# Kernel tuning notes

Hardware: AMD Instinct MI355X
Metric: run time of the kernel (lower is better)

Reference implementation:

```python
import jax, jax.numpy as jnp
import numpy as np

N = 50000      # nodes
E = 800000     # edges (avg degree 16)
IN = 128       # in_feats
H = 8          # num_heads
EMB = 32       # attention embedding dim (mode != 'cross')
OUT = 16       # out_feats per head
EF = 7         # edge (bond) feature dim


def setup_inputs() -> dict:
    key = jax.random.key(0)
    ks = jax.random.split(key, 12)
    s = 0.05  # xavier-ish scale
    return {
        "feat": jax.random.normal(ks[0], (N, IN), jnp.float32),
        "bond": jax.random.uniform(ks[1], (E, EF), jnp.float32),
        "src": jax.random.randint(ks[2], (E,), 0, N, jnp.int32),
        "dst": jax.random.randint(ks[3], (E,), 0, N, jnp.int32),
        "Wq": jax.random.normal(ks[4], (IN, H * EMB), jnp.float32) * s,
        "Wk": jax.random.normal(ks[5], (IN, H * EMB), jnp.float32) * s,
        "Wv": jax.random.normal(ks[6], (IN, H * OUT), jnp.float32) * s,
        "Wek": jax.random.normal(ks[7], (EF, H * EMB), jnp.float32) * s,
        "bek": jnp.zeros((H * EMB,), jnp.float32),
        "Wefc": jax.random.normal(ks[8], (EF, H * OUT), jnp.float32) * s,
        "befc": jnp.zeros((H * OUT,), jnp.float32),
        "bias": jnp.zeros((H * OUT,), jnp.float32),
    }


def reference(feat, bond, src, dst, Wq, Wk, Wv, Wek, bek, Wefc, befc, bias):
    n = feat.shape[0]
    # node projections
    q = (feat @ Wq).reshape(n, H, EMB)      # query
    k = (feat @ Wk).reshape(n, H, EMB)      # key
    v = (feat @ Wv).reshape(n, H, OUT)      # ft (values)
    # per-edge key from bond features
    ek = (bond @ Wek + bek).reshape(-1, H, EMB)
    # mode 'add': e = sum((q[u] + k[v]) * edge_key) over embedding dim  -> [E, H]
    e = ((q[src] + k[dst]) * ek).sum(axis=-1)
    # edge_softmax: segment softmax over incoming edges per destination node
    m = jax.ops.segment_max(e, dst, num_segments=n)          # [N, H]
    ex = jnp.exp(e - m[dst])
    denom = jax.ops.segment_sum(ex, dst, num_segments=n)     # [N, H]
    a = ex / denom[dst]                                      # [E, H]
    # per-edge feature projection
    ef = (bond @ Wefc + befc).reshape(-1, H, OUT)
    # message = ft[src] * edge_feat * a, aggregated by sum at dst
    msg = v[src] * ef * a[:, :, None]                        # [E, H, OUT]
    rst = jax.ops.segment_sum(msg, dst, num_segments=n)      # [N, H, OUT]
    rst = rst + bias.reshape(1, H, OUT)
    return rst
```

## Files before the change

kernel.cpp:

```cpp
#include <hip/hip_runtime.h>
#include <hip/hip_bf16.h>

#define HD   8
#define EMBD 32
#define OUTF 16
#define EFD  7
#define INFD 128
#define QKD  256
#define VOD  128
#define GQD  64
#define CAPMAX 64
#define NB   8
#define MAXSLOT 512
#define PBROW 524

typedef __attribute__((ext_vector_type(8))) short short8;
typedef __attribute__((ext_vector_type(4))) float f32x4;

__device__ __forceinline__ float b2f(unsigned short u) {
    return __uint_as_float(((unsigned int)u) << 16);
}
__device__ __forceinline__ unsigned short f2b(float f) {
    __hip_bfloat16 h = __float2bfloat16(f);
    return __builtin_bit_cast(unsigned short, h);
}
__device__ __forceinline__ unsigned short f2h(float f) {
    return __builtin_bit_cast(unsigned short, (_Float16)f);
}
__device__ __forceinline__ float h2f(unsigned short u) {
    return (float)__builtin_bit_cast(_Float16, u);
}

__global__ __launch_bounds__(256) void setup_kernel(
    const float* __restrict__ Wq, const float* __restrict__ Wk,
    const float* __restrict__ Wv, const float* __restrict__ Wek,
    const float* __restrict__ bek, unsigned short* __restrict__ GwT,
    int* __restrict__ counts, int N)
{
    const int b = blockIdx.x, t = threadIdx.x;
    if (b >= 16) {
        int i = (b - 16) * 256 + t;
        int stride = (gridDim.x - 16) * 256;
        for (; i < N; i += stride) counts[i] = 0;
        return;
    }
    if (b >= 8) {
        #pragma unroll
        for (int k = 0; k < 8; k++) {
            int i = (b - 8) * 2048 + k * 256 + t;
            int r = i >> 7, c = i & 127;
            GwT[(size_t)(128 + c) * 128 + r] = f2b(Wv[(size_t)r * VOD + c]);
        }
        return;
    }
    __shared__ float sWek[EFD * QKD];
    __shared__ float sbek[QKD];
    for (int i = t; i < EFD * QKD; i += 256) sWek[i] = Wek[i];
    for (int i = t; i < QKD; i += 256) sbek[i] = bek[i];
    __syncthreads();

    const int p = b * 256 + t;
    const int side = p >> 10;
    const int r = (p >> 3) & 127;
    const int h = p & 7;
    const float* W = side ? Wk : Wq;
    float wrow[EMBD];
    #pragma unroll
    for (int d = 0; d < EMBD; d++) wrow[d] = W[(size_t)r * QKD + h * EMBD + d];
    #pragma unroll
    for (int f = 0; f < EFD; f++) {
        float m = 0.f;
        #pragma unroll
        for (int d = 0; d < EMBD; d++) m += wrow[d] * sWek[f * QKD + h * EMBD + d];
        GwT[(size_t)(side * 64 + h * 8 + f) * 128 + r] = f2b(m);
    }
    float mb = 0.f;
    #pragma unroll
    for (int d = 0; d < EMBD; d++) mb += wrow[d] * sbek[h * EMBD + d];
    GwT[(size_t)(side * 64 + h * 8 + 7) * 128 + r] = f2b(mb);
}

__global__ __launch_bounds__(256) void work_kernel(
    const float* __restrict__ feat, const unsigned short* __restrict__ GwT,
    unsigned short* __restrict__ gq, unsigned short* __restrict__ gk,
    unsigned short* __restrict__ v_bf, int M,
    const int* __restrict__ src, const int* __restrict__ dst,
    const float* __restrict__ bond, int E,
    int* __restrict__ counts, short8* __restrict__ edata, int cap, int pg)
{
    if ((int)blockIdx.x >= pg) {
        int i = (blockIdx.x - pg) * 256 + threadIdx.x;
        int stride = (gridDim.x - pg) * 256;
        for (; i < E; i += stride) {
            int d = dst[i];
            const float* bp = bond + (size_t)i * EFD;
            short8 rec;
            rec[0] = (short)(unsigned short)src[i];
            #pragma unroll
            for (int f = 0; f < EFD; f++) rec[1 + f] = (short)f2b(bp[f]);
            int p = atomicAdd(&counts[d], 1);
            if (p < cap) edata[(size_t)d * cap + p] = rec;
        }
        return;
    }
    const int wave = threadIdx.x >> 6, lane = threadIdx.x & 63;
    const int quad = lane >> 4, l16 = lane & 15;
    const int m0 = blockIdx.x * 64 + wave * 16;
    const int mrow = m0 + l16;
    const int arow = (mrow < M) ? mrow : 0;

    f32x4 acc[16];
    #pragma unroll
    for (int ct = 0; ct < 16; ct++) acc[ct] = (f32x4){0.f, 0.f, 0.f, 0.f};

    #pragma unroll
    for (int ks = 0; ks < 4; ks++) {
        const float* fp = feat + (size_t)arow * INFD + ks * 32 + quad * 8;
        float4 f0 = *(const float4*)(fp);
        float4 f1 = *(const float4*)(fp + 4);
        short8 a;
        a[0] = (short)f2b(f0.x); a[1] = (short)f2b(f0.y);
        a[2] = (short)f2b(f0.z); a[3] = (short)f2b(f0.w);
        a[4] = (short)f2b(f1.x); a[5] = (short)f2b(f1.y);
        a[6] = (short)f2b(f1.z); a[7] = (short)f2b(f1.w);
        #pragma unroll
        for (int ct = 0; ct < 16; ct++) {
            short8 b = *(const short8*)(GwT + (size_t)(ct * 16 + l16) * 128 + ks * 32 + quad * 8);
            acc[ct] = __builtin_amdgcn_mfma_f32_16x16x32_bf16(a, b, acc[ct], 0, 0, 0);
        }
    }

    const int mt = m0 + quad * 4;
    #pragma unroll
    for (int ct = 0; ct < 16; ct++) {
        int nn = ct * 16 + l16;
        unsigned short* outp; int nc, ldo;
        if (ct < 4)      { outp = gq;   nc = nn;       ldo = GQD; }
        else if (ct < 8) { outp = gk;   nc = nn - 64;  ldo = GQD; }
        else             { outp = v_bf; nc = nn - 128; ldo = VOD; }
        #pragma unroll
        for (int r = 0; r < 4; r++) {
            int mm = mt + r;
            if (mm < M) outp[(size_t)mm * ldo + nc] = f2b(acc[ct][r]);
        }
    }
}

__global__ __launch_bounds__(256) void aggregate_kernel(
    const short8* __restrict__ edata,
    const unsigned short* __restrict__ gq,
    const unsigned short* __restrict__ gk,
    const unsigned short* __restrict__ v_bf,
    const int* __restrict__ counts,
    const float* __restrict__ Wefc,
    const float* __restrict__ befc,
    const float* __restrict__ bias,
    float* __restrict__ out, int N, int cap)
{
    __shared__ __align__(16) unsigned short sBond[MAXSLOT][8];
    __shared__ __align__(8)  unsigned short sS[MAXSLOT];
    __shared__ unsigned char sNode[MAXSLOT];
    __shared__ __align__(16) unsigned short sGK[NB * GQD];
    __shared__ __align__(16) unsigned short sPh[8 * PBROW];
    __shared__ float sL[NB * 8];
    __shared__ int sCnt[NB], sR16[NB], sBase[NB], sTot;

    const int t  = threadIdx.x;
    const int n0 = blockIdx.x * NB;
    const int wv = t >> 6;
    const int l  = t & 63;
    const int lrow = l & 15;
    const int lhi  = l >> 4;
    const int c0 = wv * 32 + 2 * lrow;
    const int h0 = c0 >> 4;

    short8 Bfr[2]; float bout[2];
    #pragma unroll
    for (int j = 0; j < 2; j++) {
        short8 b = {0,0,0,0,0,0,0,0};
        float bo = 0.f;
        if (lhi == 0) {
            const int c = c0 + j;
            #pragma unroll
            for (int f = 0; f < EFD; f++) b[f] = (short)f2b(Wefc[f * VOD + c]);
            b[7] = (short)f2b(befc[c]);
            bo = bias[c];
        }
        Bfr[j] = b; bout[j] = bo;
    }

    if (t < 64) {
        int c = 0;
        if (t < NB) {
            int n = n0 + t;
            c = (n < N) ? min(counts[n], cap) : 0;
        }
        int r16 = (c + 15) & ~15;
        int pre = 0;
        #pragma unroll
        for (int j = 0; j < NB; j++) {
            int vj = __shfl(r16, j, 64);
            pre += (j < t) ? vj : 0;
        }
        if (t < NB) {
            sCnt[t] = c; sR16[t] = r16; sBase[t] = pre;
            if (t == NB - 1) sTot = pre + r16;
        }
    }
    {
        const unsigned gi = (unsigned)n0 * 32u + (unsigned)t;
        if (gi < (unsigned)N * 32u)
            ((unsigned*)sGK)[t] = ((const unsigned*)gk)[gi];
    }
    __syncthreads();

    const int tot = sTot;
    {
        const int b1 = sBase[1], b2 = sBase[2], b3 = sBase[3], b4 = sBase[4],
                  b5 = sBase[5], b6 = sBase[6], b7 = sBase[7];
        for (int i = t; i < tot; i += 256) {
            int nn = (i >= b1) + (i >= b2) + (i >= b3) + (i >= b4)
                   + (i >= b5) + (i >= b6) + (i >= b7);
            int el = i - sBase[nn];
            int cnt = sCnt[nn];
            unsigned short sv = 0;
            short8 st = {0,0,0,0,0,0,0,0};
            if (el < cnt) {
                short8 r = edata[(size_t)(n0 + nn) * cap + el];
                sv = (unsigned short)r[0];
                #pragma unroll
                for (int f = 0; f < EFD; f++) st[f] = r[1 + f];
                st[7] = (short)0x3F80;
            }
            sS[i] = sv;
            sNode[i] = (unsigned char)nn;
            *(short8*)&sBond[i][0] = st;
        }
    }
    __syncthreads();

    for (int idx = t; idx < tot * 8; idx += 256) {
        const int sl = idx >> 3, lh = idx & 7;
        short8 bb = *(const short8*)&sBond[sl][0];
        float ex = 0.f;
        if (bb[7]) {
            const int nn = sNode[sl];
            short8 gv = *(const short8*)(gq + (size_t)sS[sl] * GQD + lh * 8);
            short8 kb = *(const short8*)&sGK[nn * GQD + lh * 8];
            float lv = b2f((unsigned short)gv[7]) + b2f((unsigned short)kb[7]);
            #pragma unroll
            for (int f = 0; f < EFD; f++)
                lv += b2f((unsigned short)bb[f]) *
                      (b2f((unsigned short)gv[f]) + b2f((unsigned short)kb[f]));
            ex = __expf(lv);
        }
        sPh[lh * PBROW + sl] = f2h(ex);
    }
    __syncthreads();

    {
        const int nn = t >> 5, h = (t >> 2) & 7, sub = t & 3;
        const int base = sBase[nn], cnt = sCnt[nn];
        float s = 0.f;
        for (int e = sub; e < cnt; e += 4)
            s += h2f(sPh[h * PBROW + base + e]);
        s += __shfl_xor(s, 1, 64);
        s += __shfl_xor(s, 2, 64);
        if (sub == 0) sL[nn * 8 + h] = s;
    }
    __syncthreads();

    for (int nn = 0; nn < NB; nn++) {
        const int n = n0 + nn;
        if (n >= N) break;
        const int r16 = sR16[nn];
        const int sb  = sBase[nn];
        float a0 = 0.f, a1 = 0.f;
        for (int mt = 0; mt < (r16 >> 4); mt++) {
            short8 A = {0,0,0,0,0,0,0,0};
            if (lhi == 0) A = *(const short8*)&sBond[sb + mt * 16 + lrow][0];
            const int e0 = sb + mt * 16 + lhi * 4;
            const unsigned long long sw = *(const unsigned long long*)&sS[e0];
            const unsigned s0 = (unsigned)(sw & 0xffff), s1 = (unsigned)((sw >> 16) & 0xffff);
            const unsigned s2 = (unsigned)((sw >> 32) & 0xffff), s3 = (unsigned)(sw >> 48);
            const unsigned long long pw = *(const unsigned long long*)&sPh[h0 * PBROW + e0];
            const float p0 = h2f((unsigned short)(pw & 0xffff));
            const float p1 = h2f((unsigned short)((pw >> 16) & 0xffff));
            const float p2 = h2f((unsigned short)((pw >> 32) & 0xffff));
            const float p3 = h2f((unsigned short)(pw >> 48));
            const unsigned w0 = *(const unsigned*)(v_bf + s0 * VOD + c0);
            const unsigned w1 = *(const unsigned*)(v_bf + s1 * VOD + c0);
            const unsigned w2 = *(const unsigned*)(v_bf + s2 * VOD + c0);
            const unsigned w3 = *(const unsigned*)(v_bf + s3 * VOD + c0);
            const f32x4 C0 = __builtin_amdgcn_mfma_f32_16x16x32_bf16(
                A, Bfr[0], (f32x4){0.f, 0.f, 0.f, 0.f}, 0, 0, 0);
            const f32x4 C1 = __builtin_amdgcn_mfma_f32_16x16x32_bf16(
                A, Bfr[1], (f32x4){0.f, 0.f, 0.f, 0.f}, 0, 0, 0);
            a0 = fmaf(p0 * C0[0], __uint_as_float(w0 << 16), a0);
            a1 = fmaf(p0 * C1[0], __uint_as_float(w0 & 0xffff0000u), a1);
            a0 = fmaf(p1 * C0[1], __uint_as_float(w1 << 16), a0);
            a1 = fmaf(p1 * C1[1], __uint_as_float(w1 & 0xffff0000u), a1);
            a0 = fmaf(p2 * C0[2], __uint_as_float(w2 << 16), a0);
            a1 = fmaf(p2 * C1[2], __uint_as_float(w2 & 0xffff0000u), a1);
            a0 = fmaf(p3 * C0[3], __uint_as_float(w3 << 16), a0);
            a1 = fmaf(p3 * C1[3], __uint_as_float(w3 & 0xffff0000u), a1);
        }
        a0 += __shfl_xor(a0, 16, 64);
        a0 += __shfl_xor(a0, 32, 64);
        a1 += __shfl_xor(a1, 16, 64);
        a1 += __shfl_xor(a1, 32, 64);
        if (lhi == 0) {
            const float L = sL[nn * 8 + h0];
            const float iv = (L > 0.f) ? 1.f / L : 0.f;
            float2 o;
            o.x = a0 * iv + bout[0];
            o.y = a1 * iv + bout[1];
            *(float2*)&out[(size_t)n * VOD + c0] = o;
        }
    }
}

extern "C" void kernel_launch(void* const* d_in, const int* in_sizes, int n_in,
                              void* d_out, int out_size, void* d_ws, size_t ws_size,
                              hipStream_t stream) {
    const float* feat = (const float*)d_in[0];
    const float* bond = (const float*)d_in[1];
    const int* src  = (const int*)d_in[2];
    const int* dst  = (const int*)d_in[3];
    const float* Wq   = (const float*)d_in[4];
    const float* Wk   = (const float*)d_in[5];
    const float* Wv   = (const float*)d_in[6];
    const float* Wek  = (const float*)d_in[7];
    const float* bek  = (const float*)d_in[8];
    const float* Wefc = (const float*)d_in[9];
    const float* befc = (const float*)d_in[10];
    const float* bias = (const float*)d_in[11];

    const int N = in_sizes[0] / INFD;
    const int E = in_sizes[2];

    size_t off = 0;
    auto carve = [&](size_t bytes) -> void* {
        void* p = (char*)d_ws + off;
        off += (bytes + 255) & ~(size_t)255;
        return p;
    };
    unsigned short* GwT  = (unsigned short*)carve((size_t)256 * 128 * 2);
    unsigned short* gq   = (unsigned short*)carve((size_t)N * GQD * 2);
    unsigned short* gk   = (unsigned short*)carve((size_t)N * GQD * 2);
    unsigned short* v_bf = (unsigned short*)carve((size_t)N * VOD * 2);
    int* counts    = (int*)carve((size_t)N * 4);

    size_t remain = (ws_size > off) ? (ws_size - off) : 0;
    int cap = (int)(remain / ((size_t)N * 16));
    if (cap > 64) cap = 64;
    if (cap > CAPMAX) cap = CAPMAX;
    if (cap < 1) cap = 1;
    short8* edata = (short8*)carve((size_t)N * cap * 16);

    setup_kernel<<<80, 256, 0, stream>>>(Wq, Wk, Wv, Wek, bek, GwT, counts, N);

    const int pg = (N + 63) / 64;
    work_kernel<<<pg + 3072, 256, 0, stream>>>(feat, GwT, gq, gk, v_bf, N,
                                               src, dst, bond, E, counts, edata, cap, pg);

    aggregate_kernel<<<(N + NB - 1) / NB, 256, 0, stream>>>(
        edata, gq, gk, v_bf, counts, Wefc, befc, bias, (float*)d_out, N, cap);
}
```

Before: 254.2 us.

## Partition edge scatter by XCC-owned destination ranges with dynamic chunk queues

Each scatter block reads its XCC id from a hardware register and works through 8 destination-node ranges, starting with the range tied to its own XCC. Within a range it takes edge chunks from a per-range atomic work pointer and handles only edges whose destination falls in that range. The goal is to keep atomics and writes to counts and edata local to one XCC's L2, cutting cross-die coherence traffic. The cost is that every edge's dst is read 8 times, plus extra work-pointer atomics and block-level syncs.

```diff
diff --git a/kernel.cpp b/kernel.cpp
--- a/kernel.cpp
+++ b/kernel.cpp
@@ -13,6 +13,9 @@
 #define NB   8
 #define MAXSLOT 512
 #define PBROW 524
+#define SCB  2048
+#define CHUNK 2048
+#define XCC_GETREG_IMM (20 | (31 << 11))
 
 typedef __attribute__((ext_vector_type(8))) short short8;
 typedef __attribute__((ext_vector_type(4))) float f32x4;
@@ -35,13 +38,13 @@
     const float* __restrict__ Wq, const float* __restrict__ Wk,
     const float* __restrict__ Wv, const float* __restrict__ Wek,
     const float* __restrict__ bek, unsigned short* __restrict__ GwT,
-    int* __restrict__ counts, int N)
+    int* __restrict__ counts, int NZ)
 {
     const int b = blockIdx.x, t = threadIdx.x;
     if (b >= 16) {
         int i = (b - 16) * 256 + t;
         int stride = (gridDim.x - 16) * 256;
-        for (; i < N; i += stride) counts[i] = 0;
+        for (; i < NZ; i += stride) counts[i] = 0;
         return;
     }
     if (b >= 8) {
@@ -86,20 +89,35 @@
     unsigned short* __restrict__ v_bf, int M,
     const int* __restrict__ src, const int* __restrict__ dst,
     const float* __restrict__ bond, int E,
-    int* __restrict__ counts, short8* __restrict__ edata, int cap, int pg)
+    int* __restrict__ counts, int* __restrict__ workPtr,
+    short8* __restrict__ edata, int cap, int pg)
 {
     if ((int)blockIdx.x >= pg) {
-        int i = (blockIdx.x - pg) * 256 + threadIdx.x;
-        int stride = (gridDim.x - pg) * 256;
-        for (; i < E; i += stride) {
-            int d = dst[i];
-            const float* bp = bond + (size_t)i * EFD;
-            short8 rec;
-            rec[0] = (short)(unsigned short)src[i];
-            #pragma unroll
-            for (int f = 0; f < EFD; f++) rec[1 + f] = (short)f2b(bp[f]);
-            int p = atomicAdd(&counts[d], 1);
-            if (p < cap) edata[(size_t)d * cap + p] = rec;
+        __shared__ int sChunk;
+        unsigned xcc = (unsigned)__builtin_amdgcn_s_getreg(XCC_GETREG_IMM) & 7u;
+        for (int qi = 0; qi < 8; qi++) {
+            const int q  = (int)((xcc + (unsigned)qi) & 7u);
+            const int lo = (int)(((long long)q * M) >> 3);
+            const int hi = (int)(((long long)(q + 1) * M) >> 3);
+            while (true) {
+                if (threadIdx.x == 0) sChunk = atomicAdd(&workPtr[q], CHUNK);
+                __syncthreads();
+                const int base = sChunk;
+                __syncthreads();
+                if (base >= E) break;
+                const int end = (base + CHUNK < E) ? base + CHUNK : E;
+                for (int i = base + (int)threadIdx.x; i < end; i += 256) {
+                    int d = dst[i];
+                    if (d < lo || d >= hi) continue;
+                    const float* bp = bond + (size_t)i * EFD;
+                    short8 rec;
+                    rec[0] = (short)(unsigned short)src[i];
+                    #pragma unroll
+                    for (int f = 0; f < EFD; f++) rec[1 + f] = (short)f2b(bp[f]);
+                    int p = atomicAdd(&counts[d], 1);
+                    if (p < cap) edata[(size_t)d * cap + p] = rec;
+                }
+            }
         }
         return;
     }
@@ -349,7 +367,8 @@
     unsigned short* gq   = (unsigned short*)carve((size_t)N * GQD * 2);
     unsigned short* gk   = (unsigned short*)carve((size_t)N * GQD * 2);
     unsigned short* v_bf = (unsigned short*)carve((size_t)N * VOD * 2);
-    int* counts    = (int*)carve((size_t)N * 4);
+    int* counts    = (int*)carve((size_t)(N + 64) * 4);
+    int* workPtr   = counts + N;
 
     size_t remain = (ws_size > off) ? (ws_size - off) : 0;
     int cap = (int)(remain / ((size_t)N * 16));
@@ -358,11 +377,12 @@
     if (cap < 1) cap = 1;
     short8* edata = (short8*)carve((size_t)N * cap * 16);
 
-    setup_kernel<<<80, 256, 0, stream>>>(Wq, Wk, Wv, Wek, bek, GwT, counts, N);
+    setup_kernel<<<80, 256, 0, stream>>>(Wq, Wk, Wv, Wek, bek, GwT, counts, N + 64);
 
     const int pg = (N + 63) / 64;
-    work_kernel<<<pg + 3072, 256, 0, stream>>>(feat, GwT, gq, gk, v_bf, N,
-                                               src, dst, bond, E, counts, edata, cap, pg);
+    work_kernel<<<pg + SCB, 256, 0, stream>>>(feat, GwT, gq, gk, v_bf, N,
+                                              src, dst, bond, E, counts, workPtr,
+                                              edata, cap, pg);
 
     aggregate_kernel<<<(N + NB - 1) / NB, 256, 0, stream>>>(
         edata, gq, gk, v_bf, counts, Wefc, befc, bias, (float*)d_out, N, cap);
```

Measured after the change: 443.7 us. 74.5% more time.

## Fuse attention logit and softmax denominator into aggregation MFMA loop

Applied to the files above, without the earlier changes.

Drops the separate shared-memory phases that computed per-edge exp logits into an fp16 buffer and reduced per-node denominators. Each lane now recomputes the exp logit for its head inside the main aggregation loop, gathering gq rows directly, and accumulates the denominator alongside the message sums. This removes two block barriers and about 8KB of LDS, and keeps the exp values in fp32 instead of fp16. In exchange, each logit is recomputed by the 16 lanes that share a head, and the gq gathers are repeated across those lanes.

```diff
diff --git a/kernel.cpp b/kernel.cpp
--- a/kernel.cpp
+++ b/kernel.cpp
@@ -12,7 +12,7 @@
 #define CAPMAX 64
 #define NB   8
 #define MAXSLOT 512
-#define PBROW 524
+#define SCB  3072
 
 typedef __attribute__((ext_vector_type(8))) short short8;
 typedef __attribute__((ext_vector_type(4))) float f32x4;
@@ -23,12 +23,6 @@
 __device__ __forceinline__ unsigned short f2b(float f) {
     __hip_bfloat16 h = __float2bfloat16(f);
     return __builtin_bit_cast(unsigned short, h);
-}
-__device__ __forceinline__ unsigned short f2h(float f) {
-    return __builtin_bit_cast(unsigned short, (_Float16)f);
-}
-__device__ __forceinline__ float h2f(unsigned short u) {
-    return (float)__builtin_bit_cast(_Float16, u);
 }
 
 __global__ __launch_bounds__(256) void setup_kernel(
@@ -159,10 +153,7 @@
 {
     __shared__ __align__(16) unsigned short sBond[MAXSLOT][8];
     __shared__ __align__(8)  unsigned short sS[MAXSLOT];
-    __shared__ unsigned char sNode[MAXSLOT];
     __shared__ __align__(16) unsigned short sGK[NB * GQD];
-    __shared__ __align__(16) unsigned short sPh[8 * PBROW];
-    __shared__ float sL[NB * 8];
     __shared__ int sCnt[NB], sR16[NB], sBase[NB], sTot;
 
     const int t  = threadIdx.x;
@@ -233,40 +224,8 @@
                 st[7] = (short)0x3F80;
             }
             sS[i] = sv;
-            sNode[i] = (unsigned char)nn;
             *(short8*)&sBond[i][0] = st;
         }
-    }
-    __syncthreads();
-
-    for (int idx = t; idx < tot * 8; idx += 256) {
-        const int sl = idx >> 3, lh = idx & 7;
-        short8 bb = *(const short8*)&sBond[sl][0];
-        float ex = 0.f;
-        if (bb[7]) {
-            const int nn = sNode[sl];
-            short8 gv = *(const short8*)(gq + (size_t)sS[sl] * GQD + lh * 8);
-            short8 kb = *(const short8*)&sGK[nn * GQD + lh * 8];
-            float lv = b2f((unsigned short)gv[7]) + b2f((unsigned short)kb[7]);
-            #pragma unroll
-            for (int f = 0; f < EFD; f++)
-                lv += b2f((unsigned short)bb[f]) *
-                      (b2f((unsigned short)gv[f]) + b2f((unsigned short)kb[f]));
-            ex = __expf(lv);
-        }
-        sPh[lh * PBROW + sl] = f2h(ex);
-    }
-    __syncthreads();
-
-    {
-        const int nn = t >> 5, h = (t >> 2) & 7, sub = t & 3;
-        const int base = sBase[nn], cnt = sCnt[nn];
-        float s = 0.f;
-        for (int e = sub; e < cnt; e += 4)
-            s += h2f(sPh[h * PBROW + base + e]);
-        s += __shfl_xor(s, 1, 64);
-        s += __shfl_xor(s, 2, 64);
-        if (sub == 0) sL[nn * 8 + h] = s;
     }
     __syncthreads();
 
@@ -275,7 +234,13 @@
         if (n >= N) break;
         const int r16 = sR16[nn];
         const int sb  = sBase[nn];
-        float a0 = 0.f, a1 = 0.f;
+        float kbl[8];
+        {
+            short8 kb = *(const short8*)&sGK[nn * GQD + h0 * 8];
+            #pragma unroll
+            for (int j = 0; j < 8; j++) kbl[j] = b2f((unsigned short)kb[j]);
+        }
+        float a0 = 0.f, a1 = 0.f, den = 0.f;
         for (int mt = 0; mt < (r16 >> 4); mt++) {
             short8 A = {0,0,0,0,0,0,0,0};
             if (lhi == 0) A = *(const short8*)&sBond[sb + mt * 16 + lrow][0];
@@ -283,11 +248,10 @@
             const unsigned long long sw = *(const unsigned long long*)&sS[e0];
             const unsigned s0 = (unsigned)(sw & 0xffff), s1 = (unsigned)((sw >> 16) & 0xffff);
             const unsigned s2 = (unsigned)((sw >> 32) & 0xffff), s3 = (unsigned)(sw >> 48);
-            const unsigned long long pw = *(const unsigned long long*)&sPh[h0 * PBROW + e0];
-            const float p0 = h2f((unsigned short)(pw & 0xffff));
-            const float p1 = h2f((unsigned short)((pw >> 16) & 0xffff));
-            const float p2 = h2f((unsigned short)((pw >> 32) & 0xffff));
-            const float p3 = h2f((unsigned short)(pw >> 48));
+            const short8 g0 = *(const short8*)(gq + (size_t)s0 * GQD + h0 * 8);
+            const short8 g1 = *(const short8*)(gq + (size_t)s1 * GQD + h0 * 8);
+            const short8 g2 = *(const short8*)(gq + (size_t)s2 * GQD + h0 * 8);
+            const short8 g3 = *(const short8*)(gq + (size_t)s3 * GQD + h0 * 8);
             const unsigned w0 = *(const unsigned*)(v_bf + s0 * VOD + c0);
             const unsigned w1 = *(const unsigned*)(v_bf + s1 * VOD + c0);
             const unsigned w2 = *(const unsigned*)(v_bf + s2 * VOD + c0);
@@ -296,22 +260,33 @@
                 A, Bfr[0], (f32x4){0.f, 0.f, 0.f, 0.f}, 0, 0, 0);
             const f32x4 C1 = __builtin_amdgcn_mfma_f32_16x16x32_bf16(
                 A, Bfr[1], (f32x4){0.f, 0.f, 0.f, 0.f}, 0, 0, 0);
-            a0 = fmaf(p0 * C0[0], __uint_as_float(w0 << 16), a0);
-            a1 = fmaf(p0 * C1[0], __uint_as_float(w0 & 0xffff0000u), a1);
-            a0 = fmaf(p1 * C0[1], __uint_as_float(w1 << 16), a0);
-            a1 = fmaf(p1 * C1[1], __uint_as_float(w1 & 0xffff0000u), a1);
-            a0 = fmaf(p2 * C0[2], __uint_as_float(w2 << 16), a0);
-            a1 = fmaf(p2 * C1[2], __uint_as_float(w2 & 0xffff0000u), a1);
-            a0 = fmaf(p3 * C0[3], __uint_as_float(w3 << 16), a0);
-            a1 = fmaf(p3 * C1[3], __uint_as_float(w3 & 0xffff0000u), a1);
-        }
-        a0 += __shfl_xor(a0, 16, 64);
-        a0 += __shfl_xor(a0, 32, 64);
-        a1 += __shfl_xor(a1, 16, 64);
-        a1 += __shfl_xor(a1, 32, 64);
+            #define EDGE(j, gj, wj)                                                   \
+            {                                                                         \
+                short8 bb = *(const short8*)&sBond[e0 + j][0];                        \
+                float lv = b2f((unsigned short)gj[7]) + kbl[7];                       \
+                _Pragma("unroll")                                                     \
+                for (int f = 0; f < EFD; f++)                                         \
+                    lv += b2f((unsigned short)bb[f]) *                                \
+                          (b2f((unsigned short)gj[f]) + kbl[f]);                      \
+                float p = b2f((unsigned short)bb[7]) * __expf(lv);                    \
+                den += p;                                                             \
+                a0 = fmaf(p * C0[j], __uint_as_float(wj << 16), a0);                  \
+                a1 = fmaf(p * C1[j], __uint_as_float(wj & 0xffff0000u), a1);          \
+            }
+            EDGE(0, g0, w0)
+            EDGE(1, g1, w1)
+            EDGE(2, g2, w2)
+            EDGE(3, g3, w3)
+            #undef EDGE
+        }
+        a0  += __shfl_xor(a0, 16, 64);
+        a0  += __shfl_xor(a0, 32, 64);
+        a1  += __shfl_xor(a1, 16, 64);
+        a1  += __shfl_xor(a1, 32, 64);
+        den += __shfl_xor(den, 16, 64);
+        den += __shfl_xor(den, 32, 64);
         if (lhi == 0) {
-            const float L = sL[nn * 8 + h0];
-            const float iv = (L > 0.f) ? 1.f / L : 0.f;
+            const float iv = (den > 0.f) ? 1.f / den : 0.f;
             float2 o;
             o.x = a0 * iv + bout[0];
             o.y = a1 * iv + bout[1];
@@ -361,8 +336,8 @@
     setup_kernel<<<80, 256, 0, stream>>>(Wq, Wk, Wv, Wek, bek, GwT, counts, N);
 
     const int pg = (N + 63) / 64;
-    work_kernel<<<pg + 3072, 256, 0, stream>>>(feat, GwT, gq, gk, v_bf, N,
-                                               src, dst, bond, E, counts, edata, cap, pg);
+    work_kernel<<<pg + SCB, 256, 0, stream>>>(feat, GwT, gq, gk, v_bf, N,
+                                              src, dst, bond, E, counts, edata, cap, pg);
 
     aggregate_kernel<<<(N + NB - 1) / NB, 256, 0, stream>>>(
         edata, gq, gk, v_bf, counts, Wefc, befc, bias, (float*)d_out, N, cap);
```

New measurement: 298.5 us. 17.4% more time.

## Two-level bucketed scatter of edge records to cut global atomic contention

Applied to the files above, without the earlier changes.

Edge bucketing now runs in two passes. First, records are appended to coarse bins of 64 destination nodes using one global atomic per bin. A new kernel then redistributes each bin into per-node slots using shared-memory atomics and writes the final counts. This targets scattered random global writes and per-node global atomics, but adds an extra pass over all edge records and a fixed bin capacity of 1280 that silently drops edges when a bin overflows. The hot per-bin global atomics may also contend more than the old per-node ones.

```diff
diff --git a/kernel.cpp b/kernel.cpp
--- a/kernel.cpp
+++ b/kernel.cpp
@@ -13,6 +13,10 @@
 #define NB   8
 #define MAXSLOT 512
 #define PBROW 524
+#define SCB  3072
+#define BKSH 6
+#define BKN  64
+#define BINCAP 1280
 
 typedef __attribute__((ext_vector_type(8))) short short8;
 typedef __attribute__((ext_vector_type(4))) float f32x4;
@@ -35,13 +39,13 @@
     const float* __restrict__ Wq, const float* __restrict__ Wk,
     const float* __restrict__ Wv, const float* __restrict__ Wek,
     const float* __restrict__ bek, unsigned short* __restrict__ GwT,
-    int* __restrict__ counts, int N)
+    int* __restrict__ counts, int NZ)
 {
     const int b = blockIdx.x, t = threadIdx.x;
     if (b >= 16) {
         int i = (b - 16) * 256 + t;
         int stride = (gridDim.x - 16) * 256;
-        for (; i < N; i += stride) counts[i] = 0;
+        for (; i < NZ; i += stride) counts[i] = 0;
         return;
     }
     if (b >= 8) {
@@ -86,7 +90,8 @@
     unsigned short* __restrict__ v_bf, int M,
     const int* __restrict__ src, const int* __restrict__ dst,
     const float* __restrict__ bond, int E,
-    int* __restrict__ counts, short8* __restrict__ edata, int cap, int pg)
+    int* __restrict__ binCnt, short8* __restrict__ binrec,
+    unsigned char* __restrict__ binDst, int pg)
 {
     if ((int)blockIdx.x >= pg) {
         int i = (blockIdx.x - pg) * 256 + threadIdx.x;
@@ -98,8 +103,12 @@
             rec[0] = (short)(unsigned short)src[i];
             #pragma unroll
             for (int f = 0; f < EFD; f++) rec[1 + f] = (short)f2b(bp[f]);
-            int p = atomicAdd(&counts[d], 1);
-            if (p < cap) edata[(size_t)d * cap + p] = rec;
+            int b = d >> BKSH;
+            int pos = atomicAdd(&binCnt[b], 1);
+            if (pos < BINCAP) {
+                binrec[(size_t)b * BINCAP + pos] = rec;
+                binDst[(size_t)b * BINCAP + pos] = (unsigned char)(d & (BKN - 1));
+            }
         }
         return;
     }
@@ -143,6 +152,32 @@
             int mm = mt + r;
             if (mm < M) outp[(size_t)mm * ldo + nc] = f2b(acc[ct][r]);
         }
+    }
+}
+
+__global__ __launch_bounds__(256) void scatter2_kernel(
+    const short8* __restrict__ binrec, const unsigned char* __restrict__ binDst,
+    const int* __restrict__ binCnt, short8* __restrict__ edata,
+    int* __restrict__ counts, int N, int cap)
+{
+    __shared__ int lcnt[BKN];
+    const int t = threadIdx.x, b = blockIdx.x;
+    if (t < BKN) lcnt[t] = 0;
+    __syncthreads();
+    const int cnt = min(binCnt[b], BINCAP);
+    for (int i = t; i < cnt; i += 256) {
+        short8 rec = binrec[(size_t)b * BINCAP + i];
+        int dl = (int)binDst[(size_t)b * BINCAP + i];
+        int p = atomicAdd(&lcnt[dl], 1);
+        if (p < cap) {
+            int node = (b << BKSH) + dl;
+            edata[(size_t)node * cap + p] = rec;
+        }
+    }
+    __syncthreads();
+    if (t < BKN) {
+        int node = (b << BKSH) + t;
+        if (node < N) counts[node] = lcnt[t];
     }
 }
 
@@ -338,6 +373,7 @@
 
     const int N = in_sizes[0] / INFD;
     const int E = in_sizes[2];
+    const int NBUCK = (N + BKN - 1) >> BKSH;
 
     size_t off = 0;
     auto carve = [&](size_t bytes) -> void* {
@@ -349,20 +385,28 @@
     unsigned short* gq   = (unsigned short*)carve((size_t)N * GQD * 2);
     unsigned short* gk   = (unsigned short*)carve((size_t)N * GQD * 2);
     unsigned short* v_bf = (unsigned short*)carve((size_t)N * VOD * 2);
-    int* counts    = (int*)carve((size_t)N * 4);
+    int* counts  = (int*)carve((size_t)(N + NBUCK) * 4);
+    int* binCnt  = counts + N;
+    short8* binrec = (short8*)carve((size_t)NBUCK * BINCAP * 16);
+    unsigned char* binDst = (unsigned char*)carve((size_t)NBUCK * BINCAP);
 
     size_t remain = (ws_size > off) ? (ws_size - off) : 0;
     int cap = (int)(remain / ((size_t)N * 16));
     if (cap > 64) cap = 64;
     if (cap > CAPMAX) cap = CAPMAX;
-    if (cap < 1) cap = 1;
+    cap &= ~3;
+    if (cap < 4) cap = 4;
     short8* edata = (short8*)carve((size_t)N * cap * 16);
 
-    setup_kernel<<<80, 256, 0, stream>>>(Wq, Wk, Wv, Wek, bek, GwT, counts, N);
+    setup_kernel<<<80, 256, 0, stream>>>(Wq, Wk, Wv, Wek, bek, GwT, counts, N + NBUCK);
 
     const int pg = (N + 63) / 64;
-    work_kernel<<<pg + 3072, 256, 0, stream>>>(feat, GwT, gq, gk, v_bf, N,
-                                               src, dst, bond, E, counts, edata, cap, pg);
+    work_kernel<<<pg + SCB, 256, 0, stream>>>(feat, GwT, gq, gk, v_bf, N,
+                                              src, dst, bond, E,
+                                              binCnt, binrec, binDst, pg);
+
+    scatter2_kernel<<<NBUCK, 256, 0, stream>>>(binrec, binDst, binCnt,
+                                               edata, counts, N, cap);
 
     aggregate_kernel<<<(N + NB - 1) / NB, 256, 0, stream>>>(
         edata, gq, gk, v_bf, counts, Wefc, befc, bias, (float*)d_out, N, cap);
```

After: 399.9 us. 1.57x slower.
